# Performance work log

Measured on AMD Instinct MI355X. Metric: run time of the kernel, lower is better.

## Reference

```python
import jax, jax.numpy as jnp
import numpy as np

N_NODES = 100000
N_EDGES = 2000000
F_IN = 32
HID = 32
N_CLASS = 40


def _gru_cell(m, h, wih, whh, bih, bhh):
    # torch.nn.GRUCell math; wih/whh: [3H, H_in], gates ordered r, z, n
    gi = m @ wih.T + bih
    gh = h @ whh.T + bhh
    i_r, i_z, i_n = jnp.split(gi, 3, axis=-1)
    h_r, h_z, h_n = jnp.split(gh, 3, axis=-1)
    r = jax.nn.sigmoid(i_r + h_r)
    z = jax.nn.sigmoid(i_z + h_z)
    n = jnp.tanh(i_n + r * h_n)
    return (1.0 - z) * n + z * h


def _gated_conv(x, edge_index, edge_weight, w_proj, w_msg, wih, whh, bih, bhh):
    h = x @ w_proj                                   # [N, out]
    msg = (h @ w_msg)[edge_index[0]] * edge_weight[:, None]  # gather src -> [E, out]
    agg = jax.ops.segment_sum(msg, edge_index[1], num_segments=N_NODES)  # scatter-add to dst
    return _gru_cell(agg, h, wih, whh, bih, bhh)


def setup_inputs() -> dict:
    key = jax.random.key(0)
    ks = jax.random.split(key, 16)
    s = 0.1
    return {
        "x": jax.random.normal(ks[0], (N_NODES, F_IN), jnp.float32),
        "edge_index": jax.random.randint(ks[1], (2, N_EDGES), 0, N_NODES, jnp.int64),
        "edge_weight": jax.random.uniform(ks[2], (N_EDGES,), jnp.float32),
        "W1_proj": jax.random.normal(ks[3], (F_IN, HID), jnp.float32) * s,
        "W1_msg": jax.random.normal(ks[4], (HID, HID), jnp.float32) * s,
        "gru1_wih": jax.random.normal(ks[5], (3 * HID, HID), jnp.float32) * s,
        "gru1_whh": jax.random.normal(ks[6], (3 * HID, HID), jnp.float32) * s,
        "gru1_bih": jax.random.normal(ks[7], (3 * HID,), jnp.float32) * s,
        "gru1_bhh": jax.random.normal(ks[8], (3 * HID,), jnp.float32) * s,
        "W2_proj": jax.random.normal(ks[9], (HID, N_CLASS), jnp.float32) * s,
        "W2_msg": jax.random.normal(ks[10], (N_CLASS, N_CLASS), jnp.float32) * s,
        "gru2_wih": jax.random.normal(ks[11], (3 * N_CLASS, N_CLASS), jnp.float32) * s,
        "gru2_whh": jax.random.normal(ks[12], (3 * N_CLASS, N_CLASS), jnp.float32) * s,
        "gru2_bih": jax.random.normal(ks[13], (3 * N_CLASS,), jnp.float32) * s,
        "gru2_bhh": jax.random.normal(ks[14], (3 * N_CLASS,), jnp.float32) * s,
    }


def reference(x, edge_index, edge_weight, W1_proj, W1_msg, gru1_wih, gru1_whh,
              gru1_bih, gru1_bhh, W2_proj, W2_msg, gru2_wih, gru2_whh,
              gru2_bih, gru2_bhh):
    # eval mode: dropout is identity
    h = _gated_conv(x, edge_index, edge_weight, W1_proj, W1_msg,
                    gru1_wih, gru1_whh, gru1_bih, gru1_bhh)
    h = jax.nn.relu(h)
    h = _gated_conv(h, edge_index, edge_weight, W2_proj, W2_msg,
                    gru2_wih, gru2_whh, gru2_bih, gru2_bhh)
    return jax.nn.log_softmax(h, axis=-1)
```

## Files before the change

### kernel.cpp

```cpp
#include <hip/hip_runtime.h>
#include <math.h>

#define NN 100000
#define NE 2000000
#define FIN 32
#define H 32
#define NC 40

#define NBK 196
#define BSH 9
#define CAP 10880
#define EPT 16
#define EPB (256 * EPT)

#define NPROJ 12500
#define NCT1 10
#define NCT2 12
#define NWB 118

typedef _Float16 half_t;
typedef __attribute__((ext_vector_type(8))) _Float16 half8;
typedef __attribute__((ext_vector_type(4))) float f32x4;
typedef long long ll2 __attribute__((ext_vector_type(2)));

__device__ __forceinline__ float sigm_(float x) {
    return 1.0f / (1.0f + __expf(-x));
}
__device__ __forceinline__ float tanh_(float x) {
    x = fminf(fmaxf(x, -20.0f), 20.0f);
    float e = __expf(2.0f * x);
    return (e - 1.0f) / (e + 1.0f);
}

__device__ __forceinline__ void agg_run(int n, int q,
                                        const int* __restrict__ ofs,
                                        const int* __restrict__ ocn,
                                        const int2* __restrict__ evs,
                                        const half_t* __restrict__ src,
                                        float* acc) {
    const half8* s8 = (const half8*)src + q;
    const long long* ev8 = (const long long*)evs;
    int e = ofs[n];
    int e1 = e + ocn[n];
    if ((e & 1) && e < e1) {
        long long r = __builtin_nontemporal_load(ev8 + e);
        float w = __int_as_float((int)(r >> 32));
        half8 hv = s8[(size_t)(r & 0x1FFFF) * 4];
#pragma unroll
        for (int t = 0; t < 8; ++t) acc[t] += w * (float)hv[t];
        ++e;
    }
    int nfull = (e1 - e) >> 3;
    if (nfull > 0) {
        ll2 p0 = __builtin_nontemporal_load((const ll2*)(ev8 + e));
        ll2 p1 = __builtin_nontemporal_load((const ll2*)(ev8 + e + 2));
        ll2 p2 = __builtin_nontemporal_load((const ll2*)(ev8 + e + 4));
        ll2 p3 = __builtin_nontemporal_load((const ll2*)(ev8 + e + 6));
        for (int it = 1; it < nfull; ++it) {
            int en = e + it * 8;
            ll2 q0 = __builtin_nontemporal_load((const ll2*)(ev8 + en));
            ll2 q1 = __builtin_nontemporal_load((const ll2*)(ev8 + en + 2));
            ll2 q2 = __builtin_nontemporal_load((const ll2*)(ev8 + en + 4));
            ll2 q3 = __builtin_nontemporal_load((const ll2*)(ev8 + en + 6));
            half8 h0 = s8[(size_t)(p0[0] & 0x1FFFF) * 4];
            half8 h1 = s8[(size_t)(p0[1] & 0x1FFFF) * 4];
            half8 h2 = s8[(size_t)(p1[0] & 0x1FFFF) * 4];
            half8 h3 = s8[(size_t)(p1[1] & 0x1FFFF) * 4];
            half8 h4 = s8[(size_t)(p2[0] & 0x1FFFF) * 4];
            half8 h5 = s8[(size_t)(p2[1] & 0x1FFFF) * 4];
            half8 h6 = s8[(size_t)(p3[0] & 0x1FFFF) * 4];
            half8 h7 = s8[(size_t)(p3[1] & 0x1FFFF) * 4];
            float w0 = __int_as_float((int)(p0[0] >> 32));
            float w1 = __int_as_float((int)(p0[1] >> 32));
            float w2 = __int_as_float((int)(p1[0] >> 32));
            float w3 = __int_as_float((int)(p1[1] >> 32));
            float w4 = __int_as_float((int)(p2[0] >> 32));
            float w5 = __int_as_float((int)(p2[1] >> 32));
            float w6 = __int_as_float((int)(p3[0] >> 32));
            float w7 = __int_as_float((int)(p3[1] >> 32));
#pragma unroll
            for (int t = 0; t < 8; ++t) {
                acc[t] += w0 * (float)h0[t];
                acc[t] += w1 * (float)h1[t];
                acc[t] += w2 * (float)h2[t];
                acc[t] += w3 * (float)h3[t];
                acc[t] += w4 * (float)h4[t];
                acc[t] += w5 * (float)h5[t];
                acc[t] += w6 * (float)h6[t];
                acc[t] += w7 * (float)h7[t];
            }
            p0 = q0;
            p1 = q1;
            p2 = q2;
            p3 = q3;
        }
        {
            half8 h0 = s8[(size_t)(p0[0] & 0x1FFFF) * 4];
            half8 h1 = s8[(size_t)(p0[1] & 0x1FFFF) * 4];
            half8 h2 = s8[(size_t)(p1[0] & 0x1FFFF) * 4];
            half8 h3 = s8[(size_t)(p1[1] & 0x1FFFF) * 4];
            half8 h4 = s8[(size_t)(p2[0] & 0x1FFFF) * 4];
            half8 h5 = s8[(size_t)(p2[1] & 0x1FFFF) * 4];
            half8 h6 = s8[(size_t)(p3[0] & 0x1FFFF) * 4];
            half8 h7 = s8[(size_t)(p3[1] & 0x1FFFF) * 4];
            float w0 = __int_as_float((int)(p0[0] >> 32));
            float w1 = __int_as_float((int)(p0[1] >> 32));
            float w2 = __int_as_float((int)(p1[0] >> 32));
            float w3 = __int_as_float((int)(p1[1] >> 32));
            float w4 = __int_as_float((int)(p2[0] >> 32));
            float w5 = __int_as_float((int)(p2[1] >> 32));
            float w6 = __int_as_float((int)(p3[0] >> 32));
            float w7 = __int_as_float((int)(p3[1] >> 32));
#pragma unroll
            for (int t = 0; t < 8; ++t) {
                acc[t] += w0 * (float)h0[t];
                acc[t] += w1 * (float)h1[t];
                acc[t] += w2 * (float)h2[t];
                acc[t] += w3 * (float)h3[t];
                acc[t] += w4 * (float)h4[t];
                acc[t] += w5 * (float)h5[t];
                acc[t] += w6 * (float)h6[t];
                acc[t] += w7 * (float)h7[t];
            }
        }
        e += nfull * 8;
    }
    if (e + 4 <= e1) {
        ll2 p0 = __builtin_nontemporal_load((const ll2*)(ev8 + e));
        ll2 p1 = __builtin_nontemporal_load((const ll2*)(ev8 + e + 2));
        half8 h0 = s8[(size_t)(p0[0] & 0x1FFFF) * 4];
        half8 h1 = s8[(size_t)(p0[1] & 0x1FFFF) * 4];
        half8 h2 = s8[(size_t)(p1[0] & 0x1FFFF) * 4];
        half8 h3 = s8[(size_t)(p1[1] & 0x1FFFF) * 4];
        float w0 = __int_as_float((int)(p0[0] >> 32));
        float w1 = __int_as_float((int)(p0[1] >> 32));
        float w2 = __int_as_float((int)(p1[0] >> 32));
        float w3 = __int_as_float((int)(p1[1] >> 32));
#pragma unroll
        for (int t = 0; t < 8; ++t) {
            acc[t] += w0 * (float)h0[t];
            acc[t] += w1 * (float)h1[t];
            acc[t] += w2 * (float)h2[t];
            acc[t] += w3 * (float)h3[t];
        }
        e += 4;
    }
    if (e + 2 <= e1) {
        ll2 p0 = __builtin_nontemporal_load((const ll2*)(ev8 + e));
        half8 h0 = s8[(size_t)(p0[0] & 0x1FFFF) * 4];
        half8 h1 = s8[(size_t)(p0[1] & 0x1FFFF) * 4];
        float w0 = __int_as_float((int)(p0[0] >> 32));
        float w1 = __int_as_float((int)(p0[1] >> 32));
#pragma unroll
        for (int t = 0; t < 8; ++t) {
            acc[t] += w0 * (float)h0[t];
            acc[t] += w1 * (float)h1[t];
        }
        e += 2;
    }
    if (e < e1) {
        long long r = __builtin_nontemporal_load(ev8 + e);
        float w = __int_as_float((int)(r >> 32));
        half8 hv = s8[(size_t)(r & 0x1FFFF) * 4];
#pragma unroll
        for (int t = 0; t < 8; ++t) acc[t] += w * (float)hv[t];
    }
}

__global__ __launch_bounds__(256) void kA_bucket(const int* __restrict__ ei,
                                                 const float* __restrict__ ew,
                                                 int* __restrict__ gcur,
                                                 long long* __restrict__ rec) {
    __shared__ long long recs[EPB];
    __shared__ int gdst[EPB];
    __shared__ int cnt[NBK], base[NBK], sofs[NBK];
    __shared__ int ssc[256];
    int tid = threadIdx.x;
    for (int i = tid; i < NBK; i += 256) cnt[i] = 0;
    __syncthreads();
    int e0 = blockIdx.x * EPB;
    int dcache[EPT];
#pragma unroll
    for (int i = 0; i < EPT; ++i) {
        int e = e0 + i * 256 + tid;
        dcache[i] = (e < NE) ? ei[NE + e] : -1;
        if (e < NE) atomicAdd(&cnt[dcache[i] >> BSH], 1);
    }
    __syncthreads();
    int cv = (tid < NBK) ? cnt[tid] : 0;
    ssc[tid] = cv;
    __syncthreads();
    for (int off = 1; off < 256; off <<= 1) {
        int v = (tid >= off) ? ssc[tid - off] : 0;
        __syncthreads();
        ssc[tid] += v;
        __syncthreads();
    }
    if (tid < NBK) {
        sofs[tid] = ssc[tid] - cv;
        base[tid] = atomicAdd(&gcur[tid], cv);
        cnt[tid] = 0;
    }
    __syncthreads();
#pragma unroll
    for (int i = 0; i < EPT; ++i) {
        int e = e0 + i * 256 + tid;
        if (e < NE) {
            int d = dcache[i], s = ei[e];
            int b = d >> BSH;
            int r = atomicAdd(&cnt[b], 1);
            int slot = sofs[b] + r;
            int pos = base[b] + r;
            int lo = s | ((d & 511) << 17);
            recs[slot] = (long long)(unsigned)lo |
                         ((long long)__float_as_int(ew[e]) << 32);
            gdst[slot] = (pos < CAP) ? (b * CAP + pos) : -1;
        }
    }
    __syncthreads();
    int nrec = min(EPB, NE - e0);
    for (int i = tid; i < nrec; i += 256) {
        int gd = gdst[i];
        if (gd >= 0) rec[gd] = recs[i];
    }
}

__global__ __launch_bounds__(256) void kB_sort(const int* __restrict__ gcur,
                                               const int2* __restrict__ rec,
                                               int2* __restrict__ evs,
                                               int* __restrict__ ofs,
                                               int* __restrict__ ocn) {
    __shared__ int hist[2048], lofs[2048], ssc[256];
    int tid = threadIdx.x, b = blockIdx.x;
    int nb0 = b << BSH;
    int nnodes = min(512, NN - nb0);
    int cntb = min(gcur[b], CAP);
    for (int i = tid; i < 2048; i += 256) hist[i] = 0;
    __syncthreads();
    const int2* rb = rec + (size_t)b * CAP;
    for (int i = tid; i < cntb; i += 256) {
        int rx = rb[i].x;
        int bin = (((rx >> 17) & 511) << 2) | ((rx & 0x1FFFF) >> 15);
        atomicAdd(&hist[bin], 1);
    }
    __syncthreads();
    int base = tid * 8, ls = 0, lh[8];
#pragma unroll
    for (int j = 0; j < 8; ++j) {
        lh[j] = hist[base + j];
        ls += lh[j];
    }
    ssc[tid] = ls;
    __syncthreads();
    for (int off = 1; off < 256; off <<= 1) {
        int v = (tid >= off) ? ssc[tid - off] : 0;
        __syncthreads();
        ssc[tid] += v;
        __syncthreads();
    }
    int ex = ssc[tid] - ls;
#pragma unroll
    for (int j = 0; j < 8; ++j) {
        lofs[base + j] = ex;
        ex += lh[j];
    }
    __syncthreads();
    for (int l = tid; l < nnodes; l += 256) {
        int c = hist[4 * l] + hist[4 * l + 1] + hist[4 * l + 2] + hist[4 * l + 3];
        ofs[nb0 + l] = b * CAP + lofs[4 * l];
        ocn[nb0 + l] = c;
    }
    __syncthreads();
    for (int i = tid; i < 2048; i += 256) hist[i] = 0;
    __syncthreads();
    int2* eb = evs + (size_t)b * CAP;
    for (int i = tid; i < cntb; i += 256) {
        int2 r = rb[i];
        int bin = (((r.x >> 17) & 511) << 2) | ((r.x & 0x1FFFF) >> 15);
        int rk = atomicAdd(&hist[bin], 1);
        eb[lofs[bin] + rk] = make_int2(r.x & 0x1FFFF, r.y);
    }
}

__global__ __launch_bounds__(256) void k_prep(const float* __restrict__ x,
                                              const float* __restrict__ W1p,
                                              const float* __restrict__ W1m,
                                              const float* __restrict__ wih1,
                                              const float* __restrict__ whh1,
                                              const float* __restrict__ W2p,
                                              const float* __restrict__ W2m,
                                              const float* __restrict__ wih2,
                                              const float* __restrict__ whh2,
                                              half_t* __restrict__ Hd,
                                              half_t* __restrict__ W1sw,
                                              half_t* __restrict__ W2sw,
                                              half_t* __restrict__ W2pf,
                                              int* __restrict__ gcur) {
    __shared__ float sWp[FIN * H];
    __shared__ float sx[8][FIN];
    __shared__ float P2l[32 * NC];
    int b = blockIdx.x, tid = threadIdx.x;
    if (b < NPROJ) {
        for (int i = tid; i < FIN * H; i += 256) sWp[i] = W1p[i];
        int nb = b * 8;
        int nl = tid >> 5, j = tid & 31;
        int n = nb + nl;
        if (n < NN) sx[nl][j] = x[(size_t)n * FIN + j];
        __syncthreads();
        float acc = 0.f;
#pragma unroll
        for (int k = 0; k < FIN; ++k) acc += sx[nl][k] * sWp[k * H + j];
        if (n < NN) Hd[(size_t)n * 32 + j] = (half_t)acc;
        return;
    }
    int wb = b - NPROJ;
    if (wb == 0 && tid < NBK) gcur[tid] = 0;
    if (wb < 40) {
        int i = wb * 256 + tid;
        int j = i & 7, lane = (i >> 3) & 63;
        int rest = i >> 9;
        int ct = rest % NCT1, s = rest / NCT1;
        int k = s * 32 + (lane >> 4) * 8 + j;
        int col = ct * 16 + (lane & 15);
        int g = col >> 5, jj = col & 31;
        float v = 0.f;
        if (g <= 2) {
            if (k < 32) {
                float acc = 0.f;
#pragma unroll
                for (int t = 0; t < H; ++t) acc += W1m[k * H + t] * wih1[(g * H + jj) * H + t];
                v = acc;
            } else if (g < 2) {
                v = whh1[(g * H + jj) * H + (k - 32)];
            }
        } else if (g == 3) {
            if (k >= 32) v = whh1[(2 * H + jj) * H + (k - 32)];
        } else {
            if (k >= 32 && (k - 32) == jj) v = 1.f;
        }
        W1sw[i] = (half_t)v;
    } else if (wb < 112) {
        for (int e = tid; e < 32 * NC; e += 256) {
            int k = e / NC, t = e % NC;
            float a = 0.f;
#pragma unroll
            for (int u = 0; u < NC; ++u) a += W2p[k * NC + u] * W2m[u * NC + t];
            P2l[e] = a;
        }
        __syncthreads();
        int i2 = (wb - 40) * 256 + tid;
        int j = i2 & 7, lane = (i2 >> 3) & 63;
        int rest = i2 >> 9;
        int ct = rest % NCT2, s = rest / NCT2;
        int k = s * 32 + (lane >> 4) * 8 + j;
        int col = ct * 16 + (lane & 15);
        int g = col / 48, jj = col % 48;
        float v = 0.f;
        if (jj < NC) {
            if (g <= 2) {
                if (k < 32) {
                    float acc = 0.f;
#pragma unroll
                    for (int t = 0; t < NC; ++t)
                        acc += P2l[k * NC + t] * wih2[(g * NC + jj) * NC + t];
                    v = acc;
                } else if (k < 72 && g < 2) {
                    v = whh2[(g * NC + jj) * NC + (k - 32)];
                }
            } else {
                if (k >= 32 && k < 72) v = whh2[(2 * NC + jj) * NC + (k - 32)];
            }
        }
        W2sw[i2] = (half_t)v;
    } else {
        int i3 = (wb - 112) * 256 + tid;
        int j = i3 & 7, lane = (i3 >> 3) & 63, ct = i3 >> 9;
        int k = (lane >> 4) * 8 + j;
        int col = ct * 16 + (lane & 15);
        W2pf[i3] = (half_t)((col < NC) ? W2p[k * NC + col] : 0.f);
    }
}

__global__ __launch_bounds__(128, 4) void k_l1(const int* __restrict__ ofs,
                                               const int* __restrict__ ocn,
                                               const int2* __restrict__ evs,
                                               const half_t* __restrict__ Hd,
                                               const half8* __restrict__ W1sw,
                                               const float* __restrict__ bih,
                                               const float* __restrict__ bhh,
                                               half_t* __restrict__ Hh) {
    __shared__ half8 aggT[32][5];
    int tid = threadIdx.x;
    int wave = tid >> 6, lane = tid & 63;
    int m16 = lane & 15, qq = lane >> 4;
    int n0 = blockIdx.x * 32;
    int nbw = n0 + wave * 16;
    half8 a1 = ((const half8*)Hd)[(size_t)(nbw + m16) * 4 + qq];
    {
        int nl = tid >> 2, q = tid & 3;
        float acc[8] = {0.f, 0.f, 0.f, 0.f, 0.f, 0.f, 0.f, 0.f};
        agg_run(n0 + nl, q, ofs, ocn, evs, Hd, acc);
        half8 o;
#pragma unroll
        for (int t = 0; t < 8; ++t) o[t] = (half_t)acc[t];
        aggT[nl][q] = o;
    }
    __syncthreads();
    half8 a0 = aggT[wave * 16 + m16][qq];
    f32x4 macc[NCT1];
#pragma unroll
    for (int ct = 0; ct < NCT1; ++ct) macc[ct] = (f32x4){0.f, 0.f, 0.f, 0.f};
#pragma unroll
    for (int ct = 0; ct < NCT1; ++ct) {
        macc[ct] = __builtin_amdgcn_mfma_f32_16x16x32_f16(a0, W1sw[ct * 64 + lane], macc[ct], 0, 0, 0);
        macc[ct] = __builtin_amdgcn_mfma_f32_16x16x32_f16(a1, W1sw[(NCT1 + ct) * 64 + lane], macc[ct], 0, 0, 0);
    }
#pragma unroll
    for (int ct = 0; ct < 2; ++ct) {
        int j = ct * 16 + m16;
        float br = bih[j] + bhh[j];
        float bz = bih[H + j] + bhh[H + j];
        float bi = bih[2 * H + j], bh = bhh[2 * H + j];
#pragma unroll
        for (int m = 0; m < 4; ++m) {
            int node = nbw + qq * 4 + m;
            float r = sigm_(macc[ct][m] + br);
            float z = sigm_(macc[2 + ct][m] + bz);
            float ng = tanh_(macc[4 + ct][m] + bi + r * (macc[6 + ct][m] + bh));
            float hj = macc[8 + ct][m];
            float o = fmaxf((1.f - z) * ng + z * hj, 0.f);
            Hh[(size_t)node * 32 + j] = (half_t)o;
        }
    }
}

__global__ __launch_bounds__(128, 4) void k_l2(const int* __restrict__ ofs,
                                               const int* __restrict__ ocn,
                                               const int2* __restrict__ evs,
                                               const half_t* __restrict__ Hh,
                                               const half8* __restrict__ W2sw,
                                               const half8* __restrict__ W2pf,
                                               const float* __restrict__ bih,
                                               const float* __restrict__ bhh,
                                               float* __restrict__ out) {
    __shared__ half8 aggT[32][5];
    __shared__ half_t h2c[32][72];
    int tid = threadIdx.x;
    int wave = tid >> 6, lane = tid & 63;
    int m16 = lane & 15, qq = lane >> 4;
    int n0 = blockIdx.x * 32;
    int nbw = n0 + wave * 16;
    half8 ah = ((const half8*)Hh)[(size_t)(nbw + m16) * 4 + qq];
    f32x4 hC[3];
#pragma unroll
    for (int ct = 0; ct < 3; ++ct) hC[ct] = (f32x4){0.f, 0.f, 0.f, 0.f};
#pragma unroll
    for (int ct = 0; ct < 3; ++ct)
        hC[ct] = __builtin_amdgcn_mfma_f32_16x16x32_f16(ah, W2pf[ct * 64 + lane], hC[ct], 0, 0, 0);
#pragma unroll
    for (int ct = 0; ct < 3; ++ct)
#pragma unroll
        for (int m = 0; m < 4; ++m)
            h2c[wave * 16 + qq * 4 + m][ct * 16 + m16] = (half_t)hC[ct][m];
    for (int i5 = tid; i5 < 32 * 24; i5 += 128)
        h2c[i5 / 24][48 + i5 % 24] = (half_t)0.f;
    {
        int nl = tid >> 2, q = tid & 3;
        float acc[8] = {0.f, 0.f, 0.f, 0.f, 0.f, 0.f, 0.f, 0.f};
        agg_run(n0 + nl, q, ofs, ocn, evs, Hh, acc);
        half8 o;
#pragma unroll
        for (int t = 0; t < 8; ++t) o[t] = (half_t)acc[t];
        aggT[nl][q] = o;
    }
    __syncthreads();
    half8 a0 = aggT[wave * 16 + m16][qq];
    half8 a1 = *(const half8*)&h2c[wave * 16 + m16][qq * 8];
    half8 a2 = *(const half8*)&h2c[wave * 16 + m16][32 + qq * 8];
    f32x4 macc[NCT2];
#pragma unroll
    for (int ct = 0; ct < NCT2; ++ct) macc[ct] = (f32x4){0.f, 0.f, 0.f, 0.f};
#pragma unroll
    for (int ct = 0; ct < NCT2; ++ct) {
        macc[ct] = __builtin_amdgcn_mfma_f32_16x16x32_f16(a0, W2sw[ct * 64 + lane], macc[ct], 0, 0, 0);
        macc[ct] = __builtin_amdgcn_mfma_f32_16x16x32_f16(a1, W2sw[(NCT2 + ct) * 64 + lane], macc[ct], 0, 0, 0);
        macc[ct] = __builtin_amdgcn_mfma_f32_16x16x32_f16(a2, W2sw[(2 * NCT2 + ct) * 64 + lane], macc[ct], 0, 0, 0);
    }
    float v[3][4];
#pragma unroll
    for (int ct = 0; ct < 3; ++ct) {
        int j = ct * 16 + m16;
        int jc = (j < NC) ? j : (NC - 1);
        float br = bih[jc] + bhh[jc];
        float bz = bih[NC + jc] + bhh[NC + jc];
        float bi = bih[2 * NC + jc], bh = bhh[2 * NC + jc];
#pragma unroll
        for (int m = 0; m < 4; ++m) {
            float r = sigm_(macc[ct][m] + br);
            float z = sigm_(macc[3 + ct][m] + bz);
            float ng = tanh_(macc[6 + ct][m] + bi + r * (macc[9 + ct][m] + bh));
            float hj = (float)h2c[wave * 16 + qq * 4 + m][jc];
            v[ct][m] = (1.f - z) * ng + z * hj;
        }
    }
    bool v2ok = (m16 < 8);
#pragma unroll
    for (int m = 0; m < 4; ++m) {
        float mx = fmaxf(v[0][m], v[1][m]);
        if (v2ok) mx = fmaxf(mx, v[2][m]);
#pragma unroll
        for (int d = 1; d < 16; d <<= 1) mx = fmaxf(mx, __shfl_xor(mx, d));
        float se = __expf(v[0][m] - mx) + __expf(v[1][m] - mx) +
                   (v2ok ? __expf(v[2][m] - mx) : 0.f);
#pragma unroll
        for (int d = 1; d < 16; d <<= 1) se += __shfl_xor(se, d);
        float ls = mx + __logf(se);
        int node = nbw + qq * 4 + m;
        out[(size_t)node * NC + m16] = v[0][m] - ls;
        out[(size_t)node * NC + 16 + m16] = v[1][m] - ls;
        if (v2ok) out[(size_t)node * NC + 32 + m16] = v[2][m] - ls;
    }
}

extern "C" void kernel_launch(void* const* d_in, const int* in_sizes, int n_in,
                              void* d_out, int out_size, void* d_ws, size_t ws_size,
                              hipStream_t stream) {
    const float* x = (const float*)d_in[0];
    const int* ei = (const int*)d_in[1];
    const float* ew = (const float*)d_in[2];
    const float* W1p = (const float*)d_in[3];
    const float* W1m = (const float*)d_in[4];
    const float* g1wih = (const float*)d_in[5];
    const float* g1whh = (const float*)d_in[6];
    const float* g1bih = (const float*)d_in[7];
    const float* g1bhh = (const float*)d_in[8];
    const float* W2p = (const float*)d_in[9];
    const float* W2m = (const float*)d_in[10];
    const float* g2wih = (const float*)d_in[11];
    const float* g2whh = (const float*)d_in[12];
    const float* g2bih = (const float*)d_in[13];
    const float* g2bhh = (const float*)d_in[14];
    float* ws = (float*)d_ws;

    long long* rec = (long long*)ws;
    int2* evs = (int2*)(ws + 4264960);
    half_t* Hd = (half_t*)(ws + 8529920);
    half_t* Hh = (half_t*)(ws + 10130176);
    int* ofs = (int*)(ws + 11730432);
    int* ocn = (int*)(ws + 11830432);
    int* gcur = (int*)(ws + 11930432);
    half_t* W1sw = (half_t*)(ws + 11930688);
    half_t* W2sw = W1sw + 10240;
    half_t* W2pf = W2sw + 18432;
    float* out = (float*)d_out;

    k_prep<<<NPROJ + NWB, 256, 0, stream>>>(x, W1p, W1m, g1wih, g1whh,
                                            W2p, W2m, g2wih, g2whh,
                                            Hd, W1sw, W2sw, W2pf, gcur);
    kA_bucket<<<(NE + EPB - 1) / EPB, 256, 0, stream>>>(ei, ew, gcur, rec);
    kB_sort<<<NBK, 256, 0, stream>>>(gcur, (const int2*)rec, evs, ofs, ocn);
    k_l1<<<NN / 32, 128, 0, stream>>>(ofs, ocn, evs, Hd, (const half8*)W1sw,
                                      g1bih, g1bhh, Hh);
    k_l2<<<NN / 32, 128, 0, stream>>>(ofs, ocn, evs, Hh, (const half8*)W2sw,
                                      (const half8*)W2pf, g2bih, g2bhh, out);
}
```

Measured before the change: 266.2 us.

## Split each node's edge aggregation across two thread groups, halve nodes per block

Each node's incoming edge list is now split in half, with two groups of four threads each accumulating one half. The partial sums are added in shared memory before the MFMA GRU step. Blocks now cover 16 nodes instead of 32, which doubles the grid and the threads working on gather-heavy aggregation, aiming to shorten the per-thread serial edge loop and raise memory-level parallelism. The cost is that only one wave does the MFMA/GRU epilogue per block, and the partials pass through an extra fp16 rounding step before they are summed.

```diff
diff --git a/kernel.cpp b/kernel.cpp
--- a/kernel.cpp
+++ b/kernel.cpp
@@ -32,16 +32,12 @@
     return (e - 1.0f) / (e + 1.0f);
 }
 
-__device__ __forceinline__ void agg_run(int n, int q,
-                                        const int* __restrict__ ofs,
-                                        const int* __restrict__ ocn,
+__device__ __forceinline__ void agg_run(int e, int e1, int q,
                                         const int2* __restrict__ evs,
                                         const half_t* __restrict__ src,
                                         float* acc) {
     const half8* s8 = (const half8*)src + q;
     const long long* ev8 = (const long long*)evs;
-    int e = ofs[n];
-    int e1 = e + ocn[n];
     if ((e & 1) && e < e1) {
         long long r = __builtin_nontemporal_load(ev8 + e);
         float w = __int_as_float((int)(r >> 32));
@@ -389,24 +385,32 @@
                                                const float* __restrict__ bih,
                                                const float* __restrict__ bhh,
                                                half_t* __restrict__ Hh) {
-    __shared__ half8 aggT[32][5];
+    __shared__ half8 aggT[16][9];
     int tid = threadIdx.x;
-    int wave = tid >> 6, lane = tid & 63;
-    int m16 = lane & 15, qq = lane >> 4;
-    int n0 = blockIdx.x * 32;
-    int nbw = n0 + wave * 16;
-    half8 a1 = ((const half8*)Hd)[(size_t)(nbw + m16) * 4 + qq];
+    int n0 = blockIdx.x * 16;
+    half8 a1;
+    if (tid < 64) a1 = ((const half8*)Hd)[(size_t)(n0 + (tid & 15)) * 4 + (tid >> 4)];
     {
-        int nl = tid >> 2, q = tid & 3;
+        int nl = tid >> 3, s = tid & 7, g = s >> 2, q = s & 3;
+        int n = n0 + nl;
+        int s0 = ofs[n], c = ocn[n];
+        int c0 = (c + 1) >> 1;
+        int eb = g ? (s0 + c0) : s0;
+        int ee = g ? (s0 + c) : (s0 + c0);
         float acc[8] = {0.f, 0.f, 0.f, 0.f, 0.f, 0.f, 0.f, 0.f};
-        agg_run(n0 + nl, q, ofs, ocn, evs, Hd, acc);
+        agg_run(eb, ee, q, evs, Hd, acc);
         half8 o;
 #pragma unroll
         for (int t = 0; t < 8; ++t) o[t] = (half_t)acc[t];
-        aggT[nl][q] = o;
-    }
-    __syncthreads();
-    half8 a0 = aggT[wave * 16 + m16][qq];
+        aggT[nl][s] = o;
+    }
+    __syncthreads();
+    if (tid >= 64) return;
+    int lane = tid, m16 = lane & 15, qq = lane >> 4;
+    half8 pa = aggT[m16][qq], pb = aggT[m16][4 + qq];
+    half8 a0;
+#pragma unroll
+    for (int t = 0; t < 8; ++t) a0[t] = (half_t)((float)pa[t] + (float)pb[t]);
     f32x4 macc[NCT1];
 #pragma unroll
     for (int ct = 0; ct < NCT1; ++ct) macc[ct] = (f32x4){0.f, 0.f, 0.f, 0.f};
@@ -423,7 +427,7 @@
         float bi = bih[2 * H + j], bh = bhh[2 * H + j];
 #pragma unroll
         for (int m = 0; m < 4; ++m) {
-            int node = nbw + qq * 4 + m;
+            int node = n0 + qq * 4 + m;
             float r = sigm_(macc[ct][m] + br);
             float z = sigm_(macc[2 + ct][m] + bz);
             float ng = tanh_(macc[4 + ct][m] + bi + r * (macc[6 + ct][m] + bh));
@@ -443,40 +447,52 @@
                                                const float* __restrict__ bih,
                                                const float* __restrict__ bhh,
                                                float* __restrict__ out) {
-    __shared__ half8 aggT[32][5];
-    __shared__ half_t h2c[32][72];
+    __shared__ half8 aggT[16][9];
+    __shared__ half_t h2c[16][72];
     int tid = threadIdx.x;
-    int wave = tid >> 6, lane = tid & 63;
-    int m16 = lane & 15, qq = lane >> 4;
-    int n0 = blockIdx.x * 32;
-    int nbw = n0 + wave * 16;
-    half8 ah = ((const half8*)Hh)[(size_t)(nbw + m16) * 4 + qq];
-    f32x4 hC[3];
-#pragma unroll
-    for (int ct = 0; ct < 3; ++ct) hC[ct] = (f32x4){0.f, 0.f, 0.f, 0.f};
-#pragma unroll
-    for (int ct = 0; ct < 3; ++ct)
-        hC[ct] = __builtin_amdgcn_mfma_f32_16x16x32_f16(ah, W2pf[ct * 64 + lane], hC[ct], 0, 0, 0);
-#pragma unroll
-    for (int ct = 0; ct < 3; ++ct)
-#pragma unroll
-        for (int m = 0; m < 4; ++m)
-            h2c[wave * 16 + qq * 4 + m][ct * 16 + m16] = (half_t)hC[ct][m];
-    for (int i5 = tid; i5 < 32 * 24; i5 += 128)
-        h2c[i5 / 24][48 + i5 % 24] = (half_t)0.f;
+    int n0 = blockIdx.x * 16;
+    if (tid < 64) {
+        int lane = tid, m16 = lane & 15, qq = lane >> 4;
+        half8 ah = ((const half8*)Hh)[(size_t)(n0 + m16) * 4 + qq];
+        f32x4 hC[3];
+#pragma unroll
+        for (int ct = 0; ct < 3; ++ct) hC[ct] = (f32x4){0.f, 0.f, 0.f, 0.f};
+#pragma unroll
+        for (int ct = 0; ct < 3; ++ct)
+            hC[ct] = __builtin_amdgcn_mfma_f32_16x16x32_f16(ah, W2pf[ct * 64 + lane], hC[ct], 0, 0, 0);
+#pragma unroll
+        for (int ct = 0; ct < 3; ++ct)
+#pragma unroll
+            for (int m = 0; m < 4; ++m)
+                h2c[qq * 4 + m][ct * 16 + m16] = (half_t)hC[ct][m];
+    } else {
+        int t2 = tid - 64;
+        for (int i5 = t2; i5 < 16 * 24; i5 += 64)
+            h2c[i5 / 24][48 + i5 % 24] = (half_t)0.f;
+    }
     {
-        int nl = tid >> 2, q = tid & 3;
+        int nl = tid >> 3, s = tid & 7, g = s >> 2, q = s & 3;
+        int n = n0 + nl;
+        int s0 = ofs[n], c = ocn[n];
+        int c0 = (c + 1) >> 1;
+        int eb = g ? (s0 + c0) : s0;
+        int ee = g ? (s0 + c) : (s0 + c0);
         float acc[8] = {0.f, 0.f, 0.f, 0.f, 0.f, 0.f, 0.f, 0.f};
-        agg_run(n0 + nl, q, ofs, ocn, evs, Hh, acc);
+        agg_run(eb, ee, q, evs, Hh, acc);
         half8 o;
 #pragma unroll
         for (int t = 0; t < 8; ++t) o[t] = (half_t)acc[t];
-        aggT[nl][q] = o;
-    }
-    __syncthreads();
-    half8 a0 = aggT[wave * 16 + m16][qq];
-    half8 a1 = *(const half8*)&h2c[wave * 16 + m16][qq * 8];
-    half8 a2 = *(const half8*)&h2c[wave * 16 + m16][32 + qq * 8];
+        aggT[nl][s] = o;
+    }
+    __syncthreads();
+    if (tid >= 64) return;
+    int lane = tid, m16 = lane & 15, qq = lane >> 4;
+    half8 pa = aggT[m16][qq], pb = aggT[m16][4 + qq];
+    half8 a0;
+#pragma unroll
+    for (int t = 0; t < 8; ++t) a0[t] = (half_t)((float)pa[t] + (float)pb[t]);
+    half8 a1 = *(const half8*)&h2c[m16][qq * 8];
+    half8 a2 = *(const half8*)&h2c[m16][32 + qq * 8];
     f32x4 macc[NCT2];
 #pragma unroll
     for (int ct = 0; ct < NCT2; ++ct) macc[ct] = (f32x4){0.f, 0.f, 0.f, 0.f};
@@ -499,7 +515,7 @@
             float r = sigm_(macc[ct][m] + br);
             float z = sigm_(macc[3 + ct][m] + bz);
             float ng = tanh_(macc[6 + ct][m] + bi + r * (macc[9 + ct][m] + bh));
-            float hj = (float)h2c[wave * 16 + qq * 4 + m][jc];
+            float hj = (float)h2c[qq * 4 + m][jc];
             v[ct][m] = (1.f - z) * ng + z * hj;
         }
     }
@@ -515,7 +531,7 @@
 #pragma unroll
         for (int d = 1; d < 16; d <<= 1) se += __shfl_xor(se, d);
         float ls = mx + __logf(se);
-        int node = nbw + qq * 4 + m;
+        int node = n0 + qq * 4 + m;
         out[(size_t)node * NC + m16] = v[0][m] - ls;
         out[(size_t)node * NC + 16 + m16] = v[1][m] - ls;
         if (v2ok) out[(size_t)node * NC + 32 + m16] = v[2][m] - ls;
@@ -559,8 +575,8 @@
                                             Hd, W1sw, W2sw, W2pf, gcur);
     kA_bucket<<<(NE + EPB - 1) / EPB, 256, 0, stream>>>(ei, ew, gcur, rec);
     kB_sort<<<NBK, 256, 0, stream>>>(gcur, (const int2*)rec, evs, ofs, ocn);
-    k_l1<<<NN / 32, 128, 0, stream>>>(ofs, ocn, evs, Hd, (const half8*)W1sw,
+    k_l1<<<NN / 16, 128, 0, stream>>>(ofs, ocn, evs, Hd, (const half8*)W1sw,
                                       g1bih, g1bhh, Hh);
-    k_l2<<<NN / 32, 128, 0, stream>>>(ofs, ocn, evs, Hh, (const half8*)W2sw,
+    k_l2<<<NN / 16, 128, 0, stream>>>(ofs, ocn, evs, Hh, (const half8*)W2sw,
                                       (const half8*)W2pf, g2bih, g2bhh, out);
 }
```

Measured after the change: 258.3 us, median of 2. 1.03x faster.
